# Performance work log

Measured on AMD Instinct MI355X. Metric: run time of the kernel, lower is better.

Reference implementation:

```python
import jax, jax.numpy as jnp
import numpy as np

NUM_NODES = 100000
NUM_CLASS = 63  # output channels = num_class + 1 = 64
NUM_EDGES = 1600000


def setup_inputs() -> dict:
    key = jax.random.key(0)
    k1, k2, k3, k4 = jax.random.split(key, 4)
    edges = jax.random.randint(k1, (NUM_EDGES, 2), 0, NUM_NODES, dtype=jnp.int64 if jax.config.jax_enable_x64 else jnp.int32)
    weights = jax.random.uniform(k2, (NUM_EDGES,), dtype=jnp.float32)
    poss_edge = jax.random.uniform(k3, (NUM_EDGES, NUM_CLASS + 1), dtype=jnp.float32)
    # neighbour degree sums; keep away from zero for numerical sanity
    neighbours_sum = jax.random.uniform(k4, (NUM_NODES, 1), dtype=jnp.float32, minval=0.5, maxval=1.5)
    return {"edges": edges, "weights": weights, "poss_edge": poss_edge, "neighbours_sum": neighbours_sum}


def reference(edges, weights, poss_edge, neighbours_sum):
    # value = poss_edge * weights[:, None]  -> [E, C+1]
    value = poss_edge * weights[:, None]
    # scatter_add over src node index (edges[:, 0]) into [N, C+1]
    src = edges[:, 0]
    poss_node = jax.ops.segment_sum(value, src, num_segments=NUM_NODES)
    # normalize per node by neighbour weight sum ([N,1] broadcast)
    poss_node = poss_node / neighbours_sum
    return poss_node, poss_edge
```

## Files before the change

kernel.cpp:

```cpp
#include <hip/hip_runtime.h>

#define N_NODES 100000
#define N_CLASS 64
#define N_EDGES 1600000
#define CAP     80
#define OVF_MAX 1024
#define SCAN_NB 200
#define SCAN_T  256

typedef float f4 __attribute__((ext_vector_type(4)));

__device__ __forceinline__ void gather_node(
        const int* __restrict__ ids, int n, int node, int grp, int q,
        const float* __restrict__ weights,
        const float* __restrict__ poss_edge,
        const float* __restrict__ nsum,
        float* __restrict__ acc,
        float* __restrict__ pe_out) {
    f4 val = (f4)(0.0f);
    int j = 0;

    for (; j + 16 <= n; j += 16) {
        const int e0 = ids[j + grp];
        const int e1 = ids[j + 4 + grp];
        const int e2 = ids[j + 8 + grp];
        const int e3 = ids[j + 12 + grp];
        const float w0 = weights[e0], w1 = weights[e1];
        const float w2 = weights[e2], w3 = weights[e3];
        const f4 a0 = __builtin_nontemporal_load((const f4*)(poss_edge + (size_t)e0 * N_CLASS) + q);
        const f4 a1 = __builtin_nontemporal_load((const f4*)(poss_edge + (size_t)e1 * N_CLASS) + q);
        const f4 a2 = __builtin_nontemporal_load((const f4*)(poss_edge + (size_t)e2 * N_CLASS) + q);
        const f4 a3 = __builtin_nontemporal_load((const f4*)(poss_edge + (size_t)e3 * N_CLASS) + q);
        __builtin_nontemporal_store(a0, (f4*)(pe_out + (size_t)e0 * N_CLASS) + q);
        __builtin_nontemporal_store(a1, (f4*)(pe_out + (size_t)e1 * N_CLASS) + q);
        __builtin_nontemporal_store(a2, (f4*)(pe_out + (size_t)e2 * N_CLASS) + q);
        __builtin_nontemporal_store(a3, (f4*)(pe_out + (size_t)e3 * N_CLASS) + q);
        val += a0 * w0;
        val += a1 * w1;
        val += a2 * w2;
        val += a3 * w3;
    }
    for (; j + 4 <= n; j += 4) {
        const int e = ids[j + grp];
        const float w = weights[e];
        const f4 a = __builtin_nontemporal_load((const f4*)(poss_edge + (size_t)e * N_CLASS) + q);
        __builtin_nontemporal_store(a, (f4*)(pe_out + (size_t)e * N_CLASS) + q);
        val += a * w;
    }
    if (j < n && grp < n - j) {
        const int e = ids[j + grp];
        const float w = weights[e];
        const f4 a = __builtin_nontemporal_load((const f4*)(poss_edge + (size_t)e * N_CLASS) + q);
        __builtin_nontemporal_store(a, (f4*)(pe_out + (size_t)e * N_CLASS) + q);
        val += a * w;
    }

    val.x += __shfl_xor(val.x, 16); val.y += __shfl_xor(val.y, 16);
    val.z += __shfl_xor(val.z, 16); val.w += __shfl_xor(val.w, 16);
    val.x += __shfl_xor(val.x, 32); val.y += __shfl_xor(val.y, 32);
    val.z += __shfl_xor(val.z, 32); val.w += __shfl_xor(val.w, 32);

    if (grp == 0) {
        const float inv = 1.0f / nsum[node];
        f4 o = val * inv;
        *reinterpret_cast<f4*>(acc + (size_t)node * N_CLASS + q * 4) = o;
    }
}


__global__ __launch_bounds__(256) void fill_kernel(
        const int* __restrict__ edges, int* __restrict__ cnt,
        int* __restrict__ slots, int* __restrict__ ovf_cnt, int* __restrict__ ovf) {
    const int stride = gridDim.x * blockDim.x;
    const int2* e2 = (const int2*)edges;
    for (int e = blockIdx.x * blockDim.x + threadIdx.x; e < N_EDGES; e += stride) {
        const int src = e2[e].x;
        const int pos = atomicAdd(&cnt[src], 1);
        if (pos < CAP) {
            slots[src * CAP + pos] = e;
        } else {
            const int k = atomicAdd(ovf_cnt, 1);
            if (k < OVF_MAX) ovf[k] = e;
        }
    }
}

__global__ __launch_bounds__(256) void gather_padded_kernel(
        const int* __restrict__ cnt,
        const int* __restrict__ slots,
        const float* __restrict__ weights,
        const float* __restrict__ poss_edge,
        const float* __restrict__ nsum,
        float* __restrict__ acc,
        float* __restrict__ pe_out) {
    const int node = blockIdx.x * 4 + (threadIdx.x >> 6);
    const int lane = threadIdx.x & 63;
    if (node >= N_NODES) return;
    const int n = min(cnt[node], CAP);
    gather_node(slots + node * CAP, n, node, lane >> 4, lane & 15,
                weights, poss_edge, nsum, acc, pe_out);
}

__global__ void cleanup_kernel(const int* __restrict__ ovf_cnt, const int* __restrict__ ovf,
                               const int* __restrict__ edges,
                               const float* __restrict__ weights,
                               const float* __restrict__ poss_edge,
                               const float* __restrict__ nsum,
                               float* __restrict__ acc, float* __restrict__ pe_out) {
    const int m = min(*ovf_cnt, OVF_MAX);
    for (int t = threadIdx.x; t < m * 16; t += blockDim.x) {
        const int k = t >> 4, q = t & 15;
        const int e = ovf[k];
        const int src = edges[2 * e];
        const float w = weights[e];
        const f4 a = *((const f4*)(poss_edge + (size_t)e * N_CLASS) + q);
        *((f4*)(pe_out + (size_t)e * N_CLASS) + q) = a;
        const float inv = 1.0f / nsum[src];
        float* base = acc + (size_t)src * N_CLASS + q * 4;
        atomicAdd(base + 0, a.x * w * inv);
        atomicAdd(base + 1, a.y * w * inv);
        atomicAdd(base + 2, a.z * w * inv);
        atomicAdd(base + 3, a.w * w * inv);
    }
}


__global__ void hist_kernel(const int* __restrict__ edges, int* __restrict__ counts) {
    const int stride = gridDim.x * blockDim.x;
    const int2* e2 = (const int2*)edges;
    for (int e = blockIdx.x * blockDim.x + threadIdx.x; e < N_EDGES; e += stride)
        atomicAdd(&counts[e2[e].x], 1);
}

__global__ void scanA_kernel(const int* __restrict__ counts, int* __restrict__ bsum) {
    __shared__ int s[SCAN_T];
    const int b = blockIdx.x, t = threadIdx.x;
    const int i0 = b * 512 + 2 * t;
    int c0 = (i0     < N_NODES) ? counts[i0]     : 0;
    int c1 = (i0 + 1 < N_NODES) ? counts[i0 + 1] : 0;
    s[t] = c0 + c1;
    __syncthreads();
    for (int d = SCAN_T / 2; d > 0; d >>= 1) {
        if (t < d) s[t] += s[t + d];
        __syncthreads();
    }
    if (t == 0) bsum[b] = s[0];
}

__global__ void scanB_kernel(int* __restrict__ bsum, int* __restrict__ offsets) {
    __shared__ int s[SCAN_T];
    const int t = threadIdx.x;
    const int v = (t < SCAN_NB) ? bsum[t] : 0;
    s[t] = v;
    __syncthreads();
    for (int d = 1; d < SCAN_T; d <<= 1) {
        int x = (t >= d) ? s[t - d] : 0;
        __syncthreads();
        s[t] += x;
        __syncthreads();
    }
    if (t < SCAN_NB) bsum[t] = s[t] - v;
    if (t == SCAN_T - 1) offsets[N_NODES] = s[t];
}

__global__ void scanC_kernel(int* __restrict__ offsets, const int* __restrict__ bsum,
                             int* __restrict__ cursor) {
    __shared__ int s[SCAN_T];
    const int b = blockIdx.x, t = threadIdx.x;
    const int i0 = b * 512 + 2 * t;
    int c0 = (i0     < N_NODES) ? offsets[i0]     : 0;
    int c1 = (i0 + 1 < N_NODES) ? offsets[i0 + 1] : 0;
    const int pair = c0 + c1;
    s[t] = pair;
    __syncthreads();
    for (int d = 1; d < SCAN_T; d <<= 1) {
        int x = (t >= d) ? s[t - d] : 0;
        __syncthreads();
        s[t] += x;
        __syncthreads();
    }
    const int excl = s[t] - pair + bsum[b];
    if (i0 < N_NODES)     { offsets[i0]     = excl;      cursor[i0]     = excl; }
    if (i0 + 1 < N_NODES) { offsets[i0 + 1] = excl + c0; cursor[i0 + 1] = excl + c0; }
}

__global__ void place_kernel(const int* __restrict__ edges,
                             int* __restrict__ cursor,
                             int* __restrict__ edge_ids) {
    const int stride = gridDim.x * blockDim.x;
    const int2* e2 = (const int2*)edges;
    for (int e = blockIdx.x * blockDim.x + threadIdx.x; e < N_EDGES; e += stride) {
        const int src = e2[e].x;
        const int pos = atomicAdd(&cursor[src], 1);
        edge_ids[pos] = e;
    }
}

__global__ __launch_bounds__(256) void gather_csr_kernel(
        const int* __restrict__ offsets,
        const int* __restrict__ edge_ids,
        const float* __restrict__ weights,
        const float* __restrict__ poss_edge,
        const float* __restrict__ nsum,
        float* __restrict__ acc,
        float* __restrict__ pe_out) {
    const int node = blockIdx.x * 4 + (threadIdx.x >> 6);
    const int lane = threadIdx.x & 63;
    if (node >= N_NODES) return;
    const int beg = offsets[node];
    const int n   = offsets[node + 1] - beg;
    gather_node(edge_ids + beg, n, node, lane >> 4, lane & 15,
                weights, poss_edge, nsum, acc, pe_out);
}

__global__ void scatter_copy_kernel(const int* __restrict__ edges,
                                    const float* __restrict__ weights,
                                    const float* __restrict__ poss_edge,
                                    float* __restrict__ acc,
                                    float* __restrict__ pe_out) {
    const int total = N_EDGES * 16;
    const int stride = gridDim.x * blockDim.x;
    for (int t = blockIdx.x * blockDim.x + threadIdx.x; t < total; t += stride) {
        const int e  = t >> 4;
        const int c0 = (t & 15) << 2;
        const float4 pe = *reinterpret_cast<const float4*>(poss_edge + (size_t)e * N_CLASS + c0);
        const float  w  = weights[e];
        const int    src = edges[2 * e];
        *reinterpret_cast<float4*>(pe_out + (size_t)e * N_CLASS + c0) = pe;
        float* a = acc + (size_t)src * N_CLASS + c0;
        atomicAdd(a + 0, pe.x * w);
        atomicAdd(a + 1, pe.y * w);
        atomicAdd(a + 2, pe.z * w);
        atomicAdd(a + 3, pe.w * w);
    }
}

__global__ void divide_kernel(float* __restrict__ acc,
                              const float* __restrict__ nsum) {
    const int t = blockIdx.x * blockDim.x + threadIdx.x;
    if (t >= N_NODES * 16) return;
    const int   node = t >> 4;
    const float d    = nsum[node];
    float4 v = *reinterpret_cast<float4*>(acc + (size_t)t * 4);
    v.x /= d; v.y /= d; v.z /= d; v.w /= d;
    *reinterpret_cast<float4*>(acc + (size_t)t * 4) = v;
}

extern "C" void kernel_launch(void* const* d_in, const int* in_sizes, int n_in,
                              void* d_out, int out_size, void* d_ws, size_t ws_size,
                              hipStream_t stream) {
    const int*   edges     = (const int*)d_in[0];
    const float* weights   = (const float*)d_in[1];
    const float* poss_edge = (const float*)d_in[2];
    const float* nsum      = (const float*)d_in[3];

    float* out    = (float*)d_out;
    float* acc    = out;
    float* pe_out = out + (size_t)N_NODES * N_CLASS;

    const size_t ws_A =
        (size_t)(N_NODES + 1 + OVF_MAX + (size_t)N_NODES * CAP) * sizeof(int);
    const size_t ws_B =
        (size_t)(N_NODES + 1 + N_NODES + 256 + N_EDGES) * sizeof(int);

    if (ws_size >= ws_A) {
        int* cnt     = (int*)d_ws;
        int* ovf_cnt = cnt + N_NODES;
        int* ovf     = ovf_cnt + 1;
        int* slots   = ovf + OVF_MAX;

        (void)hipMemsetAsync(cnt, 0, (size_t)(N_NODES + 1) * sizeof(int), stream);
        fill_kernel<<<2048, 256, 0, stream>>>(edges, cnt, slots, ovf_cnt, ovf);
        gather_padded_kernel<<<(N_NODES + 3) / 4, 256, 0, stream>>>(
            cnt, slots, weights, poss_edge, nsum, acc, pe_out);
        cleanup_kernel<<<1, 256, 0, stream>>>(
            ovf_cnt, ovf, edges, weights, poss_edge, nsum, acc, pe_out);
    } else if (ws_size >= ws_B) {
        int* offsets  = (int*)d_ws;
        int* cursor   = offsets + (N_NODES + 1);
        int* bsum     = cursor + N_NODES;
        int* edge_ids = bsum + 256;

        (void)hipMemsetAsync(offsets, 0, (size_t)N_NODES * sizeof(int), stream);
        hist_kernel <<<2048, 256, 0, stream>>>(edges, offsets);
        scanA_kernel<<<SCAN_NB, SCAN_T, 0, stream>>>(offsets, bsum);
        scanB_kernel<<<1, SCAN_T, 0, stream>>>(bsum, offsets);
        scanC_kernel<<<SCAN_NB, SCAN_T, 0, stream>>>(offsets, bsum, cursor);
        place_kernel<<<2048, 256, 0, stream>>>(edges, cursor, edge_ids);
        gather_csr_kernel<<<(N_NODES + 3) / 4, 256, 0, stream>>>(
            offsets, edge_ids, weights, poss_edge, nsum, acc, pe_out);
    } else {
        (void)hipMemsetAsync(acc, 0, (size_t)N_NODES * N_CLASS * sizeof(float), stream);
        scatter_copy_kernel<<<8192, 256, 0, stream>>>(edges, weights, poss_edge, acc, pe_out);
        const int div_threads = N_NODES * 16;
        divide_kernel<<<(div_threads + 255) / 256, 256, 0, stream>>>(acc, nsum);
    }
}
```

Before: 308.8 us.

## Move poss_edge copy into coalesced fill pass and shrink slot capacity

Fuses the copy of poss_edge to its output into the bucket-fill kernel. There each wave streams four consecutive edge rows, so the copy runs in edge order rather than through scattered per-node gather accesses. The gather kernel now only reads poss_edge to accumulate. The cost is that poss_edge is read twice, once in the fill pass and once in the gather, which raises total memory traffic. Per-node slot capacity is also reduced from 80 to 64, shrinking the slot workspace while leaving the overflow path for rare high-degree nodes.

```diff
diff --git a/kernel.cpp b/kernel.cpp
--- a/kernel.cpp
+++ b/kernel.cpp
@@ -3,23 +3,64 @@
 #define N_NODES 100000
 #define N_CLASS 64
 #define N_EDGES 1600000
-#define CAP     80
+#define CAP     64
 #define OVF_MAX 1024
 #define SCAN_NB 200
 #define SCAN_T  256
 
 typedef float f4 __attribute__((ext_vector_type(4)));
 
-__device__ __forceinline__ void gather_node(
-        const int* __restrict__ ids, int n, int node, int grp, int q,
+
+__global__ __launch_bounds__(256) void fillcopy_kernel(
+        const int* __restrict__ edges,
+        const float* __restrict__ poss_edge,
+        float* __restrict__ pe_out,
+        int* __restrict__ cnt,
+        int* __restrict__ slots,
+        int* __restrict__ ovf_cnt,
+        int* __restrict__ ovf) {
+    const int wave   = (blockIdx.x * blockDim.x + threadIdx.x) >> 6;
+    const int lane   = threadIdx.x & 63;
+    const int grp    = lane >> 4;
+    const int q      = lane & 15;
+    const int nwaves = (gridDim.x * blockDim.x) >> 6;
+    const int2* e2   = (const int2*)edges;
+
+    for (int base = wave * 4; base < N_EDGES; base += nwaves * 4) {
+        const int e = base + grp;
+        const f4 a = __builtin_nontemporal_load((const f4*)(poss_edge + (size_t)e * N_CLASS) + q);
+        __builtin_nontemporal_store(a, (f4*)(pe_out + (size_t)e * N_CLASS) + q);
+        if (q == 0) {
+            const int src = e2[e].x;
+            const int pos = atomicAdd(&cnt[src], 1);
+            if (pos < CAP) {
+                slots[src * CAP + pos] = e;
+            } else {
+                const int k = atomicAdd(ovf_cnt, 1);
+                if (k < OVF_MAX) ovf[k] = e;
+            }
+        }
+    }
+}
+
+__global__ __launch_bounds__(256) void gather_padded_kernel(
+        const int* __restrict__ cnt,
+        const int* __restrict__ slots,
         const float* __restrict__ weights,
         const float* __restrict__ poss_edge,
         const float* __restrict__ nsum,
-        float* __restrict__ acc,
-        float* __restrict__ pe_out) {
+        float* __restrict__ acc) {
+    const int node = blockIdx.x * 4 + (threadIdx.x >> 6);
+    const int lane = threadIdx.x & 63;
+    const int grp  = lane >> 4;
+    const int q    = lane & 15;
+    if (node >= N_NODES) return;
+
+    const int n = min(cnt[node], CAP);
+    const int* ids = slots + node * CAP;
+
     f4 val = (f4)(0.0f);
     int j = 0;
-
     for (; j + 16 <= n; j += 16) {
         const int e0 = ids[j + grp];
         const int e1 = ids[j + 4 + grp];
@@ -31,10 +72,6 @@
         const f4 a1 = __builtin_nontemporal_load((const f4*)(poss_edge + (size_t)e1 * N_CLASS) + q);
         const f4 a2 = __builtin_nontemporal_load((const f4*)(poss_edge + (size_t)e2 * N_CLASS) + q);
         const f4 a3 = __builtin_nontemporal_load((const f4*)(poss_edge + (size_t)e3 * N_CLASS) + q);
-        __builtin_nontemporal_store(a0, (f4*)(pe_out + (size_t)e0 * N_CLASS) + q);
-        __builtin_nontemporal_store(a1, (f4*)(pe_out + (size_t)e1 * N_CLASS) + q);
-        __builtin_nontemporal_store(a2, (f4*)(pe_out + (size_t)e2 * N_CLASS) + q);
-        __builtin_nontemporal_store(a3, (f4*)(pe_out + (size_t)e3 * N_CLASS) + q);
         val += a0 * w0;
         val += a1 * w1;
         val += a2 * w2;
@@ -42,17 +79,13 @@
     }
     for (; j + 4 <= n; j += 4) {
         const int e = ids[j + grp];
-        const float w = weights[e];
-        const f4 a = __builtin_nontemporal_load((const f4*)(poss_edge + (size_t)e * N_CLASS) + q);
-        __builtin_nontemporal_store(a, (f4*)(pe_out + (size_t)e * N_CLASS) + q);
-        val += a * w;
+        const f4 a = __builtin_nontemporal_load((const f4*)(poss_edge + (size_t)e * N_CLASS) + q);
+        val += a * weights[e];
     }
     if (j < n && grp < n - j) {
         const int e = ids[j + grp];
-        const float w = weights[e];
-        const f4 a = __builtin_nontemporal_load((const f4*)(poss_edge + (size_t)e * N_CLASS) + q);
-        __builtin_nontemporal_store(a, (f4*)(pe_out + (size_t)e * N_CLASS) + q);
-        val += a * w;
+        const f4 a = __builtin_nontemporal_load((const f4*)(poss_edge + (size_t)e * N_CLASS) + q);
+        val += a * weights[e];
     }
 
     val.x += __shfl_xor(val.x, 16); val.y += __shfl_xor(val.y, 16);
@@ -65,40 +98,6 @@
         f4 o = val * inv;
         *reinterpret_cast<f4*>(acc + (size_t)node * N_CLASS + q * 4) = o;
     }
-}
-
-
-__global__ __launch_bounds__(256) void fill_kernel(
-        const int* __restrict__ edges, int* __restrict__ cnt,
-        int* __restrict__ slots, int* __restrict__ ovf_cnt, int* __restrict__ ovf) {
-    const int stride = gridDim.x * blockDim.x;
-    const int2* e2 = (const int2*)edges;
-    for (int e = blockIdx.x * blockDim.x + threadIdx.x; e < N_EDGES; e += stride) {
-        const int src = e2[e].x;
-        const int pos = atomicAdd(&cnt[src], 1);
-        if (pos < CAP) {
-            slots[src * CAP + pos] = e;
-        } else {
-            const int k = atomicAdd(ovf_cnt, 1);
-            if (k < OVF_MAX) ovf[k] = e;
-        }
-    }
-}
-
-__global__ __launch_bounds__(256) void gather_padded_kernel(
-        const int* __restrict__ cnt,
-        const int* __restrict__ slots,
-        const float* __restrict__ weights,
-        const float* __restrict__ poss_edge,
-        const float* __restrict__ nsum,
-        float* __restrict__ acc,
-        float* __restrict__ pe_out) {
-    const int node = blockIdx.x * 4 + (threadIdx.x >> 6);
-    const int lane = threadIdx.x & 63;
-    if (node >= N_NODES) return;
-    const int n = min(cnt[node], CAP);
-    gather_node(slots + node * CAP, n, node, lane >> 4, lane & 15,
-                weights, poss_edge, nsum, acc, pe_out);
 }
 
 __global__ void cleanup_kernel(const int* __restrict__ ovf_cnt, const int* __restrict__ ovf,
@@ -106,7 +105,7 @@
                                const float* __restrict__ weights,
                                const float* __restrict__ poss_edge,
                                const float* __restrict__ nsum,
-                               float* __restrict__ acc, float* __restrict__ pe_out) {
+                               float* __restrict__ acc) {
     const int m = min(*ovf_cnt, OVF_MAX);
     for (int t = threadIdx.x; t < m * 16; t += blockDim.x) {
         const int k = t >> 4, q = t & 15;
@@ -114,7 +113,6 @@
         const int src = edges[2 * e];
         const float w = weights[e];
         const f4 a = *((const f4*)(poss_edge + (size_t)e * N_CLASS) + q);
-        *((f4*)(pe_out + (size_t)e * N_CLASS) + q) = a;
         const float inv = 1.0f / nsum[src];
         float* base = acc + (size_t)src * N_CLASS + q * 4;
         atomicAdd(base + 0, a.x * w * inv);
@@ -206,11 +204,40 @@
         float* __restrict__ pe_out) {
     const int node = blockIdx.x * 4 + (threadIdx.x >> 6);
     const int lane = threadIdx.x & 63;
+    const int grp  = lane >> 4;
+    const int q    = lane & 15;
     if (node >= N_NODES) return;
     const int beg = offsets[node];
     const int n   = offsets[node + 1] - beg;
-    gather_node(edge_ids + beg, n, node, lane >> 4, lane & 15,
-                weights, poss_edge, nsum, acc, pe_out);
+    const int* ids = edge_ids + beg;
+
+    f4 val = (f4)(0.0f);
+    int j = 0;
+    for (; j + 4 <= n; j += 4) {
+        const int e = ids[j + grp];
+        const float w = weights[e];
+        const f4 a = __builtin_nontemporal_load((const f4*)(poss_edge + (size_t)e * N_CLASS) + q);
+        __builtin_nontemporal_store(a, (f4*)(pe_out + (size_t)e * N_CLASS) + q);
+        val += a * w;
+    }
+    if (j < n && grp < n - j) {
+        const int e = ids[j + grp];
+        const float w = weights[e];
+        const f4 a = __builtin_nontemporal_load((const f4*)(poss_edge + (size_t)e * N_CLASS) + q);
+        __builtin_nontemporal_store(a, (f4*)(pe_out + (size_t)e * N_CLASS) + q);
+        val += a * w;
+    }
+
+    val.x += __shfl_xor(val.x, 16); val.y += __shfl_xor(val.y, 16);
+    val.z += __shfl_xor(val.z, 16); val.w += __shfl_xor(val.w, 16);
+    val.x += __shfl_xor(val.x, 32); val.y += __shfl_xor(val.y, 32);
+    val.z += __shfl_xor(val.z, 32); val.w += __shfl_xor(val.w, 32);
+
+    if (grp == 0) {
+        const float inv = 1.0f / nsum[node];
+        f4 o = val * inv;
+        *reinterpret_cast<f4*>(acc + (size_t)node * N_CLASS + q * 4) = o;
+    }
 }
 
 __global__ void scatter_copy_kernel(const int* __restrict__ edges,
@@ -270,11 +297,12 @@
         int* slots   = ovf + OVF_MAX;
 
         (void)hipMemsetAsync(cnt, 0, (size_t)(N_NODES + 1) * sizeof(int), stream);
-        fill_kernel<<<2048, 256, 0, stream>>>(edges, cnt, slots, ovf_cnt, ovf);
+        fillcopy_kernel<<<8192, 256, 0, stream>>>(
+            edges, poss_edge, pe_out, cnt, slots, ovf_cnt, ovf);
         gather_padded_kernel<<<(N_NODES + 3) / 4, 256, 0, stream>>>(
-            cnt, slots, weights, poss_edge, nsum, acc, pe_out);
+            cnt, slots, weights, poss_edge, nsum, acc);
         cleanup_kernel<<<1, 256, 0, stream>>>(
-            ovf_cnt, ovf, edges, weights, poss_edge, nsum, acc, pe_out);
+            ovf_cnt, ovf, edges, weights, poss_edge, nsum, acc);
     } else if (ws_size >= ws_B) {
         int* offsets  = (int*)d_ws;
         int* cursor   = offsets + (N_NODES + 1);
```

After: 276.9 us, median of 2. -10.3%, faster.
